# Optimization experiments

Hardware: AMD Instinct MI355X
Metric: run time of the kernel (lower is better)

Reference implementation:

```python
import jax, jax.numpy as jnp
import numpy as np


def pixel_coordinates(h, w):
    # (h, w, 2) grid of (x, y) in [-1, 1]
    y = jnp.linspace(-1.0, 1.0, h)
    x = jnp.linspace(-1.0, 1.0, w)
    yy, xx = jnp.meshgrid(y, x, indexing='ij')
    return jnp.stack([xx, yy], axis=-1)


def base_grid(h_in, w_in):
    y = jnp.linspace(-1.0 + 1.0 / h_in, 1.0 - 1.0 / h_in, h_in)
    x = jnp.linspace(-1.0 + 1.0 / w_in, 1.0 - 1.0 / w_in, w_in)
    yy, xx = jnp.meshgrid(y, x, indexing='ij')
    return jnp.stack([xx, yy], axis=-1)  # [h_in, w_in, 2]


def setup_inputs() -> dict:
    key = jax.random.key(0)
    params = jax.random.normal(key, (2, 9, 32, 32), dtype=jnp.float32)
    return {"params": params, "h_out": 128, "w_out": 128}


def reference(params, h_out, w_out):
    B, _, h_in, w_in = params.shape
    N = h_in * w_in
    p = jnp.transpose(params, (0, 2, 3, 1))  # [B, h_in, w_in, 9]

    # positions (mu): base grid + tanh(offset) * (2/h_in)
    mu = base_grid(h_in, w_in)[None] + jnp.tanh(p[..., 0:2]) * (2.0 / h_in)
    mu = mu.reshape(B, N, 2)

    # covariance via Cholesky-like factor L = [[exp(a), 0], [b, exp(c)]]
    v1x = jnp.exp(p[..., 2])
    v2x = p[..., 3]
    v2y = jnp.exp(p[..., 4])
    zero = jnp.zeros_like(v1x)
    L = jnp.stack([jnp.stack([v1x, zero], axis=-1),
                   jnp.stack([v2x, v2y], axis=-1)], axis=-2)  # [B,h,w,2,2]
    cov = L @ jnp.swapaxes(L, -1, -2)
    cov = cov.reshape(B, N, 2, 2) + jnp.eye(2, dtype=params.dtype) * 1e-5
    Sigma_inv = jnp.linalg.inv(cov)  # [B, N, 2, 2]

    colors = jax.nn.sigmoid(p[..., 5:8]).reshape(B, N, 3)
    opacities = jax.nn.sigmoid(p[..., 8]).reshape(B, N)

    coords = pixel_coordinates(h_out, w_out)  # [H, W, 2]
    dx = coords[None, None] - mu[:, :, None, None, :]  # [B, N, H, W, 2]
    exponent = -0.5 * jnp.einsum('bnhwi,bnij,bnhwj->bnhw', dx, Sigma_inv, dx)
    exponent = jnp.clip(exponent, -20.0, 20.0)
    kernel = jnp.exp(exponent)  # [B, N, H, W]

    weights = opacities[:, :, None, None] * kernel
    weights_sum = jnp.sum(weights, axis=1, keepdims=True) + 1e-8
    norm_w = weights / weights_sum  # [B, N, H, W]
    image = jnp.einsum('bnhw,bnc->bchw', norm_w, colors)  # [B, 3, H, W]
    return image
```

## Files before the change

kernel.cpp:

```cpp
#include <hip/hip_runtime.h>


#define NB   2
#define NG   1024
#define HOUT 128
#define WOUT 128
#define GSTRIDE 12

__global__ __launch_bounds__(256) void gauss_setup(const float* __restrict__ params,
                                                   float* __restrict__ gd) {
    int gid = blockIdx.x * blockDim.x + threadIdx.x;
    if (gid >= NB * NG) return;
    int b = gid >> 10;
    int n = gid & (NG - 1);
    int h = n >> 5;
    int w = n & 31;

    const float* P = params + b * 9 * NG + n;
    float p0 = P[0 * NG];
    float p1 = P[1 * NG];
    float p2 = P[2 * NG];
    float p3 = P[3 * NG];
    float p4 = P[4 * NG];
    float p5 = P[5 * NG];
    float p6 = P[6 * NG];
    float p7 = P[7 * NG];
    float p8 = P[8 * NG];

    float mux = -0.96875f + (float)w * 0.0625f + tanhf(p0) * 0.0625f;
    float muy = -0.96875f + (float)h * 0.0625f + tanhf(p1) * 0.0625f;

    float ea  = expf(p2);
    float ec  = expf(p4);
    float c00 = ea * ea + 1e-5f;
    float c01 = p3 * ea;
    float c11 = p3 * p3 + ec * ec + 1e-5f;
    float det = c00 * c11 - c01 * c01;
    float id  = 1.0f / det;
    float Sa  =  c11 * id;
    float Sb  = -c01 * id;
    float Sc  =  c00 * id;

    const float s = -0.72134752044448169f;
    float A  = s * Sa;
    float B2 = 2.0f * s * Sb;
    float C  = s * Sc;

    float cr = 1.0f / (1.0f + expf(-p5));
    float cg = 1.0f / (1.0f + expf(-p6));
    float cb = 1.0f / (1.0f + expf(-p7));
    float op = 1.0f / (1.0f + expf(-p8));

    float* o = gd + gid * GSTRIDE;
    o[0]  = mux;  o[1]  = muy;  o[2]  = A;       o[3]  = B2;
    o[4]  = C;    o[5]  = op;   o[6]  = op * cr; o[7]  = op * cg;
    o[8]  = op * cb; o[9] = 0.0f; o[10] = 0.0f; o[11] = 0.0f;
}

__global__ __launch_bounds__(512, 2) void gauss_render(const float* __restrict__ gd,
                                                       float* __restrict__ out) {
    __shared__ float  sg[NG * GSTRIDE];
    __shared__ float4 sred[512];

    const int tx  = threadIdx.x;
    const int ty  = threadIdx.y;
    const int tid = ty * 64 + tx;
    const int blk = blockIdx.x;
    const int b   = blk >> 8;
    const int pix = ((blk & 255) << 6) + tx;

    const float4* src = (const float4*)(gd + b * NG * GSTRIDE);
    float4* dst = (float4*)sg;
    #pragma unroll
    for (int i = tid; i < NG * GSTRIDE / 4; i += 512) dst[i] = src[i];
    __syncthreads();

    const int h = pix >> 7;
    const int w = pix & 127;
    const float px = -1.0f + (float)w * (2.0f / 127.0f);
    const float py = -1.0f + (float)h * (2.0f / 127.0f);

    float wsum = 0.0f, ar = 0.0f, ag = 0.0f, ab = 0.0f;

    const float* gp = sg + ty * (NG / 8) * GSTRIDE;
    #pragma unroll 4
    for (int j = 0; j < NG / 8; ++j) {
        const float4* q4 = (const float4*)(gp + j * GSTRIDE);
        float4 q0 = q4[0];
        float4 q1 = q4[1];
        float  q2 = ((const float*)q4)[8];

        float dx = px - q0.x;
        float dy = py - q0.y;
        float m1 = q0.z * dx;
        float m2 = q0.w * dx;
        float m3 = q1.x * dy;
        float e2 = fmaf(m1, dx, fmaf(m2, dy, m3 * dy));
        e2 = fmaxf(e2, -28.853900817779268f);
        float k = __builtin_amdgcn_exp2f(e2);

        wsum = fmaf(q1.y, k, wsum);
        ar   = fmaf(q1.z, k, ar);
        ag   = fmaf(q1.w, k, ag);
        ab   = fmaf(q2,   k, ab);
    }

    sred[tid] = make_float4(wsum, ar, ag, ab);
    __syncthreads();

    if (ty == 0) {
        float4 a = sred[tx];
        #pragma unroll
        for (int k2 = 1; k2 < 8; ++k2) {
            float4 t = sred[k2 * 64 + tx];
            a.x += t.x; a.y += t.y; a.z += t.z; a.w += t.w;
        }
        float inv = 1.0f / (a.x + 1e-8f);
        float* ob = out + b * 3 * (HOUT * WOUT) + pix;
        ob[0]                 = a.y * inv;
        ob[HOUT * WOUT]       = a.z * inv;
        ob[2 * HOUT * WOUT]   = a.w * inv;
    }
}

extern "C" void kernel_launch(void* const* d_in, const int* in_sizes, int n_in,
                              void* d_out, int out_size, void* d_ws, size_t ws_size,
                              hipStream_t stream) {
    const float* params = (const float*)d_in[0];
    float* gd  = (float*)d_ws;
    float* out = (float*)d_out;

    hipLaunchKernelGGL(gauss_setup, dim3((NB * NG + 255) / 256), dim3(256), 0, stream,
                       params, gd);
    hipLaunchKernelGGL(gauss_render, dim3(NB * (HOUT * WOUT) / 64), dim3(64, 8), 0,
                       stream, gd, out);
}
```

Baseline: 76.27 us.

## Read Gaussian parameters via wave-uniform scalar loads instead of LDS staging

Drops the per-block copy of all 1024 Gaussian records into shared memory and the barrier after it. Each wave instead reads its chunk straight from global memory, with the chunk index made wave-uniform through readfirstlane so the compiler can issue scalar loads. The quadratic form is also regrouped to use fewer multiplies. This removes the LDS fill, the sync and the LDS read traffic, and lifts the two-blocks-per-CU bound set by shared memory, but it relies on the scalar cache and on the compiler actually emitting scalar loads.

Result: faster. 74.52 us (-2.3%).

```diff
diff --git a/kernel.cpp b/kernel.cpp
--- a/kernel.cpp
+++ b/kernel.cpp
@@ -57,9 +57,8 @@
     o[8]  = op * cb; o[9] = 0.0f; o[10] = 0.0f; o[11] = 0.0f;
 }
 
-__global__ __launch_bounds__(512, 2) void gauss_render(const float* __restrict__ gd,
-                                                       float* __restrict__ out) {
-    __shared__ float  sg[NG * GSTRIDE];
+__global__ __launch_bounds__(512) void gauss_render(const float* __restrict__ gd,
+                                                    float* __restrict__ out) {
     __shared__ float4 sred[512];
 
     const int tx  = threadIdx.x;
@@ -69,40 +68,36 @@
     const int b   = blk >> 8;
     const int pix = ((blk & 255) << 6) + tx;
 
-    const float4* src = (const float4*)(gd + b * NG * GSTRIDE);
-    float4* dst = (float4*)sg;
-    #pragma unroll
-    for (int i = tid; i < NG * GSTRIDE / 4; i += 512) dst[i] = src[i];
-    __syncthreads();
-
     const int h = pix >> 7;
     const int w = pix & 127;
     const float px = -1.0f + (float)w * (2.0f / 127.0f);
     const float py = -1.0f + (float)h * (2.0f / 127.0f);
 
+    const int chunk = __builtin_amdgcn_readfirstlane(ty);
+    const float* __restrict__ gp =
+        gd + (size_t)b * NG * GSTRIDE + (size_t)chunk * (NG / 8) * GSTRIDE;
+
     float wsum = 0.0f, ar = 0.0f, ag = 0.0f, ab = 0.0f;
 
-    const float* gp = sg + ty * (NG / 8) * GSTRIDE;
     #pragma unroll 4
     for (int j = 0; j < NG / 8; ++j) {
-        const float4* q4 = (const float4*)(gp + j * GSTRIDE);
-        float4 q0 = q4[0];
-        float4 q1 = q4[1];
-        float  q2 = ((const float*)q4)[8];
+        const float* __restrict__ r = gp + j * GSTRIDE;
+        const float mux = r[0], muy = r[1];
+        const float A   = r[2], B2  = r[3], C = r[4];
+        const float op  = r[5], ocr = r[6], ocg = r[7], ocb = r[8];
 
-        float dx = px - q0.x;
-        float dy = py - q0.y;
-        float m1 = q0.z * dx;
-        float m2 = q0.w * dx;
-        float m3 = q1.x * dy;
-        float e2 = fmaf(m1, dx, fmaf(m2, dy, m3 * dy));
+        float dx = px - mux;
+        float dy = py - muy;
+        float m  = A * dx;
+        m        = fmaf(B2, dy, m);
+        float e2 = fmaf(C * dy, dy, m * dx);
         e2 = fmaxf(e2, -28.853900817779268f);
         float k = __builtin_amdgcn_exp2f(e2);
 
-        wsum = fmaf(q1.y, k, wsum);
-        ar   = fmaf(q1.z, k, ar);
-        ag   = fmaf(q1.w, k, ag);
-        ab   = fmaf(q2,   k, ab);
+        wsum = fmaf(op,  k, wsum);
+        ar   = fmaf(ocr, k, ar);
+        ag   = fmaf(ocg, k, ag);
+        ab   = fmaf(ocb, k, ab);
     }
 
     sred[tid] = make_float4(wsum, ar, ag, ab);
```
